# Kernel optimization log

Measured on AMD Instinct MI355X. Metric: run time of the kernel, lower is better.

Reference implementation:

```python
import jax, jax.numpy as jnp
import numpy as np

K = 3
TOPK = 32
TELEPORT = 0.1
LN_EPS = 1e-5


def _block(x, ln_g, ln_b, w1, b1, w2, b2, log_tau, gate):
    residual = x
    # pre: LayerNorm -> Linear -> GELU (exact erf, torch default)
    mu = jnp.mean(x, axis=-1, keepdims=True)
    var = jnp.mean(jnp.square(x - mu), axis=-1, keepdims=True)
    h = (x - mu) * jax.lax.rsqrt(var + LN_EPS) * ln_g + ln_b
    h = jax.nn.gelu(h @ w1 + b1, approximate=False)  # [B, N, H]

    # dynamic cosine adjacency with top-k sparsification
    tau = jnp.maximum(jnp.exp(log_tau), 1e-3)
    xn = h / jnp.maximum(jnp.linalg.norm(h, axis=-1, keepdims=True), 1e-12)
    A = jnp.maximum(jnp.einsum('bnf,bmf->bnm', xn, xn), 0.0)  # [B, N, N]
    B, N, _ = A.shape
    vals, idx = jax.lax.top_k(A, TOPK)  # idx: [B, N, TOPK]
    bi = jnp.arange(B)[:, None, None]
    ni = jnp.arange(N)[None, :, None]
    mask = jnp.zeros(A.shape, dtype=bool).at[bi, ni, idx].set(True)
    I = jnp.eye(N, dtype=A.dtype)
    A = jnp.where(mask, A, 0.0) + I
    A = A / tau

    # teleport + symmetric degree normalization
    A = (1.0 - TELEPORT) * A + TELEPORT * I
    deg = jnp.maximum(A.sum(-1), 1e-6)  # [B, N]
    dm12 = deg ** -0.5
    Ahat = dm12[:, :, None] * A * dm12[:, None, :]

    # Chebyshev propagation
    T0 = h
    outs = [T0]
    if K > 1:
        T1 = jnp.einsum('bnm,bmf->bnf', Ahat, T0)
        outs.append(T1)
    for _ in range(2, K):
        outs.append(2.0 * jnp.einsum('bnm,bmf->bnf', Ahat, outs[-1]) - outs[-2])
    hcat = jnp.concatenate(outs, axis=-1)  # [B, N, H*K]
    y = hcat @ w2 + b2
    return residual + jnp.tanh(gate) * y


def setup_inputs() -> dict:
    key = jax.random.key(0)
    k0, k1, k2 = jax.random.split(key, 3)
    Bsz, N, D, H, O = 4, 4096, 128, 128, 128
    x = jax.random.normal(k0, (Bsz, N, D), dtype=jnp.float32)
    ln_g = jnp.ones((D,), jnp.float32)
    ln_b = jnp.zeros((D,), jnp.float32)
    w1 = jax.random.normal(k1, (D, H), jnp.float32) / np.float32(np.sqrt(D))
    b1 = jnp.zeros((H,), jnp.float32)
    w2 = jax.random.normal(k2, (H * K, O), jnp.float32) / np.float32(np.sqrt(H * K))
    b2 = jnp.zeros((O,), jnp.float32)
    log_tau = jnp.asarray(np.log(0.5), jnp.float32)
    gate = jnp.asarray(0.2, jnp.float32)
    return {"x": x, "ln_g": ln_g, "ln_b": ln_b, "w1": w1, "b1": b1,
            "w2": w2, "b2": b2, "log_tau": log_tau, "gate": gate}


def reference(x, ln_g, ln_b, w1, b1, w2, b2, log_tau, gate):
    return _block(x, ln_g, ln_b, w1, b1, w2, b2, log_tau, gate)
```

## Files before the change

kernel.cpp:

```cpp
#include <hip/hip_runtime.h>
#include <hip/hip_bf16.h>
#include <stdint.h>

#define NB 4
#define NN 4096

using f16x8 = __attribute__((ext_vector_type(8))) _Float16;
using f32x4 = __attribute__((ext_vector_type(4))) float;

__device__ __forceinline__ float wave_sum(float v) {
  #pragma unroll
  for (int o = 32; o > 0; o >>= 1) v += __shfl_xor(v, o, 64);
  return v;
}
__device__ __forceinline__ unsigned short f2h_bits(float f) {
  _Float16 hf = (_Float16)f;
  unsigned short us;
  __builtin_memcpy(&us, &hf, 2);
  return us;
}
__device__ __forceinline__ unsigned pack2h(float lo, float hi) {
  return ((unsigned)f2h_bits(hi) << 16) | (unsigned)f2h_bits(lo);
}

#define INS16(c) do { unsigned t_;                      \
  t_ = max(l0, c);  c = min(l0, c);  l0 = t_;           \
  t_ = max(l1, c);  c = min(l1, c);  l1 = t_;           \
  t_ = max(l2, c);  c = min(l2, c);  l2 = t_;           \
  t_ = max(l3, c);  c = min(l3, c);  l3 = t_;           \
  t_ = max(l4, c);  c = min(l4, c);  l4 = t_;           \
  t_ = max(l5, c);  c = min(l5, c);  l5 = t_;           \
  t_ = max(l6, c);  c = min(l6, c);  l6 = t_;           \
  t_ = max(l7, c);  c = min(l7, c);  l7 = t_;           \
  t_ = max(l8, c);  c = min(l8, c);  l8 = t_;           \
  t_ = max(l9, c);  c = min(l9, c);  l9 = t_;           \
  t_ = max(l10, c); c = min(l10, c); l10 = t_;          \
  t_ = max(l11, c); c = min(l11, c); l11 = t_;          \
  t_ = max(l12, c); c = min(l12, c); l12 = t_;          \
  t_ = max(l13, c); c = min(l13, c); l13 = t_;          \
  t_ = max(l14, c); c = min(l14, c); l14 = t_;          \
  l15 = max(l15, c);                                    \
} while (0)

__global__ __launch_bounds__(128) void k_prepw(
    const float* __restrict__ w1, const float* __restrict__ w2,
    _Float16* __restrict__ w1t16, _Float16* __restrict__ w2t16) {
  int n = blockIdx.x;
  int t = threadIdx.x;
  __shared__ _Float16 v16[128];
  __shared__ float v[384];
  v16[t] = (_Float16)w1[(size_t)t * 128 + n];
  #pragma unroll
  for (int i = 0; i < 3; ++i) v[i * 128 + t] = w2[(size_t)(i * 128 + t) * 128 + n];
  __syncthreads();
  if (t < 16) {
    union { _Float16 hh[8]; uint4 u; } pk;
    #pragma unroll
    for (int j = 0; j < 8; ++j) pk.hh[j] = v16[t * 8 + j];
    *(uint4*)(w1t16 + (size_t)n * 128 + (size_t)(t ^ (n & 7)) * 8) = pk.u;
  }
  if (t < 48) {
    int kc = t >> 4, cl = t & 15;
    union { _Float16 hh[8]; uint4 u; } pk;
    #pragma unroll
    for (int e = 0; e < 8; ++e) pk.hh[e] = (_Float16)v[t * 8 + e];
    *(uint4*)(w2t16 + (size_t)n * 384 + kc * 128 + (size_t)(cl ^ (n & 7)) * 8) = pk.u;
  }
}

__global__ __launch_bounds__(256) void k0_ln(
    const float* __restrict__ x, const float* __restrict__ ln_g,
    const float* __restrict__ ln_b, _Float16* __restrict__ ln16) {
  int lane = threadIdx.x & 63;
  int row = blockIdx.x * 4 + (threadIdx.x >> 6);
  float2 xv = ((const float2*)x)[(size_t)row * 64 + lane];
  float2 gv = ((const float2*)ln_g)[lane];
  float2 bv = ((const float2*)ln_b)[lane];
  float mu = wave_sum(xv.x + xv.y) * (1.0f / 128.0f);
  float dx = xv.x - mu, dy = xv.y - mu;
  float var = wave_sum(dx * dx + dy * dy) * (1.0f / 128.0f);
  float ri = 1.0f / sqrtf(var + 1e-5f);
  float h0 = dx * ri * gv.x + bv.x;
  float h1 = dy * ri * gv.y + bv.y;
  int c = lane >> 2;
  int addr = row * 128 + ((c ^ (row & 7)) << 3) + (lane & 3) * 2;
  *(unsigned*)(ln16 + addr) = pack2h(h0, h1);
}

__global__ __launch_bounds__(256) void k1_mfma(
    const _Float16* __restrict__ ln16, const _Float16* __restrict__ w1t16,
    const float* __restrict__ b1, _Float16* __restrict__ h16,
    _Float16* __restrict__ hn16) {
  __shared__ _Float16 As[64 * 128];
  __shared__ _Float16 Bs[128 * 128];
  int tid = threadIdx.x;
  int lane = tid & 63;
  int wv = tid >> 6;
  int rbase = blockIdx.x * 64;
  #pragma unroll
  for (int i = 0; i < 4; ++i) {
    int idx = tid + 256 * i;
    __builtin_amdgcn_global_load_lds(
        (const __attribute__((address_space(1))) void*)(ln16 + (size_t)rbase * 128 + (size_t)idx * 8),
        (__attribute__((address_space(3))) void*)(As + (size_t)idx * 8), 16, 0, 0);
  }
  #pragma unroll
  for (int i = 0; i < 8; ++i) {
    int idx = tid + 256 * i;
    __builtin_amdgcn_global_load_lds(
        (const __attribute__((address_space(1))) void*)(w1t16 + (size_t)idx * 8),
        (__attribute__((address_space(3))) void*)(Bs + (size_t)idx * 8), 16, 0, 0);
  }
  asm volatile("s_waitcnt vmcnt(0)" ::: "memory");
  __syncthreads();

  int rl = lane & 15, kg = lane >> 4;
  f32x4 acc[8];
  #pragma unroll
  for (int j = 0; j < 8; ++j) acc[j] = (f32x4){0.f, 0.f, 0.f, 0.f};
  #pragma unroll
  for (int kk = 0; kk < 4; ++kk) {
    int cL = kk * 4 + kg;
    int r = wv * 16 + rl;
    f16x8 a = *(const f16x8*)(As + r * 128 + (cL ^ (r & 7)) * 8);
    #pragma unroll
    for (int j = 0; j < 8; ++j) {
      int n = j * 16 + rl;
      f16x8 bf = *(const f16x8*)(Bs + n * 128 + (cL ^ (n & 7)) * 8);
      acc[j] = __builtin_amdgcn_mfma_f32_16x16x32_f16(a, bf, acc[j], 0, 0, 0);
    }
  }
  float ssq[4] = {0.f, 0.f, 0.f, 0.f};
  #pragma unroll
  for (int j = 0; j < 8; ++j) {
    float bv = b1[j * 16 + rl];
    #pragma unroll
    for (int rg = 0; rg < 4; ++rg) {
      float z = acc[j][rg] + bv;
      float g = 0.5f * z * (1.0f + erff(z * 0.70710678118654752440f));
      acc[j][rg] = g;
      ssq[rg] += g * g;
    }
  }
  #pragma unroll
  for (int o = 1; o < 16; o <<= 1)
    #pragma unroll
    for (int rg = 0; rg < 4; ++rg) ssq[rg] += __shfl_xor(ssq[rg], o, 64);
  float rinv[4];
  #pragma unroll
  for (int rg = 0; rg < 4; ++rg) rinv[rg] = 1.0f / fmaxf(sqrtf(ssq[rg]), 1e-12f);

  #pragma unroll
  for (int j = 0; j < 8; ++j) {
    #pragma unroll
    for (int rg = 0; rg < 4; ++rg) {
      float g = acc[j][rg];
      float gp = __shfl_xor(g, 1, 64);
      if ((rl & 1) == 0) {
        int row = rbase + wv * 16 + kg * 4 + rg;
        int col = j * 16 + rl;
        int c = col >> 3;
        int ad = row * 128 + (((c ^ (row & 7))) << 3) + (col & 7);
        *(unsigned*)(h16 + ad) = pack2h(g, gp);
        *(unsigned*)(hn16 + ad) = pack2h(g * rinv[rg], gp * rinv[rg]);
      }
    }
  }
}

__global__ __launch_bounds__(256, 1) void k_scores_topk(
    const _Float16* __restrict__ hn16, int* __restrict__ nidx,
    float* __restrict__ nval, float* __restrict__ dm12,
    const float* __restrict__ p_log_tau) {
  __shared__ _Float16 Qs[64 * 128];
  __shared__ _Float16 Cs[2][128 * 128];
  __shared__ unsigned stk[32 * 256];
  int tid = threadIdx.x;
  int lane = tid & 63;
  int wv = tid >> 6;
  int rl = lane & 15, kg = lane >> 4;
  int blk = blockIdx.x;
  int b = blk >> 6;
  int qbase = (blk & 63) * 64;
  const _Float16* hb = hn16 + (size_t)b * NN * 128;

  #pragma unroll
  for (int i = 0; i < 4; ++i) {
    int idx = tid + 256 * i;
    __builtin_amdgcn_global_load_lds(
        (const __attribute__((address_space(1))) void*)(hb + (size_t)qbase * 128 + (size_t)idx * 8),
        (__attribute__((address_space(3))) void*)(Qs + (size_t)idx * 8), 16, 0, 0);
  }
  #pragma unroll
  for (int i = 0; i < 8; ++i) {
    int idx = tid + 256 * i;
    __builtin_amdgcn_global_load_lds(
        (const __attribute__((address_space(1))) void*)(hb + (size_t)idx * 8),
        (__attribute__((address_space(3))) void*)(Cs[0] + (size_t)idx * 8), 16, 0, 0);
  }
  asm volatile("s_waitcnt vmcnt(0)" ::: "memory");
  __syncthreads();

  int qrow = wv * 16 + rl;
  f16x8 bq[4];
  #pragma unroll
  for (int kk = 0; kk < 4; ++kk)
    bq[kk] = *(const f16x8*)(Qs + qrow * 128 + ((kk * 4 + kg) ^ (qrow & 7)) * 8);

  unsigned l0 = 0, l1 = 0, l2 = 0, l3 = 0, l4 = 0, l5 = 0, l6 = 0, l7 = 0,
           l8 = 0, l9 = 0, l10 = 0, l11 = 0, l12 = 0, l13 = 0, l14 = 0, l15 = 0;
  float thr = 0.0f;

  for (int cb = 0; cb < 32; ++cb) {
    int cur = cb & 1;
    if (cb < 31) {
      const _Float16* csrc = hb + (size_t)(cb + 1) * 128 * 128;
      #pragma unroll
      for (int i = 0; i < 8; ++i) {
        int idx = tid + 256 * i;
        __builtin_amdgcn_global_load_lds(
            (const __attribute__((address_space(1))) void*)(csrc + (size_t)idx * 8),
            (__attribute__((address_space(3))) void*)(Cs[cur ^ 1] + (size_t)idx * 8), 16, 0, 0);
      }
    }
    f32x4 acc[8];
    #pragma unroll
    for (int j = 0; j < 8; ++j) acc[j] = (f32x4){0.f, 0.f, 0.f, 0.f};
    #pragma unroll
    for (int kk = 0; kk < 4; ++kk) {
      #pragma unroll
      for (int j = 0; j < 8; ++j) {
        int mrow = j * 16 + rl;
        f16x8 a = *(const f16x8*)(Cs[cur] + mrow * 128 + ((kk * 4 + kg) ^ (rl & 7)) * 8);
        acc[j] = __builtin_amdgcn_mfma_f32_16x16x32_f16(a, bq[kk], acc[j], 0, 0, 0);
      }
    }
    int cnt = 0;
    int kb = 4095 - (cb * 128 + kg * 4);
    #pragma unroll
    for (int j = 0; j < 8; ++j) {
      float mx = fmaxf(fmaxf(acc[j][0], acc[j][1]), fmaxf(acc[j][2], acc[j][3]));
      if (mx >= thr) {
        #pragma unroll
        for (int rg = 0; rg < 4; ++rg) {
          float v = acc[j][rg];
          if (v >= thr) {
            unsigned key = (__float_as_uint(fmaxf(v, 0.0f)) & 0xFFFFF000u) |
                           (unsigned)(kb - j * 16 - rg);
            stk[cnt * 256 + tid] = key;
            ++cnt;
          }
        }
      }
    }
    for (int i = 0;; ++i) {
      if (__ballot(i < cnt) == 0ull) break;
      unsigned c = (i < cnt) ? stk[i * 256 + tid] : 0u;
      INS16(c);
    }
    thr = __uint_as_float(l15 & 0xFFFFF000u);
    asm volatile("s_waitcnt vmcnt(0)" ::: "memory");
    __syncthreads();
  }

  unsigned sv[8];
  float sum = 0.0f;
  #pragma unroll
  for (int e = 0; e < 32; ++e) {
    unsigned v = l0;
    v = max(v, (unsigned)__shfl_xor((int)v, 16, 64));
    v = max(v, (unsigned)__shfl_xor((int)v, 32, 64));
    if (l0 == v) {
      l0 = l1; l1 = l2; l2 = l3; l3 = l4; l4 = l5; l5 = l6; l6 = l7; l7 = l8;
      l8 = l9; l9 = l10; l10 = l11; l11 = l12; l12 = l13; l13 = l14; l14 = l15; l15 = 0;
    }
    sum += __uint_as_float(v & 0xFFFFF000u);
    if (kg == (e & 3)) sv[e >> 2] = v;
  }
  int grow = b * NN + qbase + qrow;
  #pragma unroll
  for (int s = 0; s < 8; ++s) {
    unsigned v = sv[s];
    nidx[(size_t)grow * 32 + s * 4 + kg] = 4095 - (int)(v & 0xFFFu);
    nval[(size_t)grow * 32 + s * 4 + kg] = __uint_as_float(v & 0xFFFFF000u);
  }
  if (kg == 0) {
    float tau = fmaxf(expf(p_log_tau[0]), 1e-3f);
    float deg = fmaxf(0.9f * ((sum + 1.0f) / tau) + 0.1f, 1e-6f);
    dm12[grow] = 1.0f / sqrtf(deg);
  }
}

__global__ __launch_bounds__(128) void k_cheb1(
    const _Float16* __restrict__ h16, const int* __restrict__ nidx,
    const float* __restrict__ nval, const float* __restrict__ dm12,
    const float* __restrict__ p_log_tau, _Float16* __restrict__ T116) {
  int row = blockIdx.x;
  int b = row >> 12;
  int tid = threadIdx.x;
  __shared__ float cj[32];
  __shared__ int mj[32];
  __shared__ float cdsh;
  float tau = fmaxf(expf(p_log_tau[0]), 1e-3f);
  float scale = 0.9f / tau;
  float dn = dm12[row];
  if (tid < 32) {
    int m = nidx[(size_t)row * 32 + tid];
    cj[tid] = scale * nval[(size_t)row * 32 + tid] * dn * dm12[b * NN + m];
    mj[tid] = m;
  }
  if (tid == 0) cdsh = (scale + 0.1f) * dn * dn;
  __syncthreads();
  int c = tid >> 3, e = tid & 7;
  const _Float16* hb = h16 + (size_t)b * NN * 128;
  float acc = cdsh * (float)h16[(size_t)row * 128 + ((c ^ (row & 7)) << 3) + e];
  #pragma unroll 8
  for (int j = 0; j < 32; ++j) {
    int m = mj[j];
    acc += cj[j] * (float)hb[(size_t)m * 128 + ((c ^ (m & 7)) << 3) + e];
  }
  float p = __shfl_xor(acc, 1, 64);
  if (!(tid & 1))
    *(unsigned*)(T116 + (size_t)row * 128 + ((c ^ (row & 7)) << 3) + e) = pack2h(acc, p);
}

__global__ __launch_bounds__(128) void k_cheb2(
    const _Float16* __restrict__ h16, const _Float16* __restrict__ T116,
    const int* __restrict__ nidx, const float* __restrict__ nval,
    const float* __restrict__ dm12, const float* __restrict__ p_log_tau,
    _Float16* __restrict__ T216) {
  int row = blockIdx.x;
  int b = row >> 12;
  int tid = threadIdx.x;
  __shared__ float cj[32];
  __shared__ int mj[32];
  __shared__ float cdsh;
  float tau = fmaxf(expf(p_log_tau[0]), 1e-3f);
  float scale = 0.9f / tau;
  float dn = dm12[row];
  if (tid < 32) {
    int m = nidx[(size_t)row * 32 + tid];
    cj[tid] = scale * nval[(size_t)row * 32 + tid] * dn * dm12[b * NN + m];
    mj[tid] = m;
  }
  if (tid == 0) cdsh = (scale + 0.1f) * dn * dn;
  __syncthreads();
  int c = tid >> 3, e = tid & 7;
  int sw_own = ((c ^ (row & 7)) << 3) + e;
  const _Float16* T1b = T116 + (size_t)b * NN * 128;
  float a = cdsh * (float)T116[(size_t)row * 128 + sw_own];
  #pragma unroll 8
  for (int j = 0; j < 32; ++j) {
    int m = mj[j];
    a += cj[j] * (float)T1b[(size_t)m * 128 + ((c ^ (m & 7)) << 3) + e];
  }
  float t2 = 2.0f * a - (float)h16[(size_t)row * 128 + sw_own];
  float p = __shfl_xor(t2, 1, 64);
  if (!(tid & 1))
    *(unsigned*)(T216 + (size_t)row * 128 + sw_own) = pack2h(t2, p);
}

__global__ __launch_bounds__(256, 1) void k_out(
    const float* __restrict__ x, const _Float16* __restrict__ h16,
    const _Float16* __restrict__ T116, const _Float16* __restrict__ T216,
    const _Float16* __restrict__ w2t16, const float* __restrict__ b2,
    const float* __restrict__ p_gate, float* __restrict__ out) {
  __shared__ _Float16 As3[3][64 * 128];
  __shared__ _Float16 Bs3[3][128 * 128];
  int tid = threadIdx.x;
  int lane = tid & 63;
  int wv = tid >> 6;
  int rbase = blockIdx.x * 64;
  const _Float16* srcs[3] = {h16, T116, T216};
  #pragma unroll
  for (int kc = 0; kc < 3; ++kc) {
    const _Float16* src = srcs[kc] + (size_t)rbase * 128;
    #pragma unroll
    for (int i = 0; i < 4; ++i) {
      int idx = tid + 256 * i;
      __builtin_amdgcn_global_load_lds(
          (const __attribute__((address_space(1))) void*)(src + (size_t)idx * 8),
          (__attribute__((address_space(3))) void*)(As3[kc] + (size_t)idx * 8), 16, 0, 0);
    }
    #pragma unroll
    for (int i = 0; i < 8; ++i) {
      int idx = tid + 256 * i;
      int n = idx >> 4, cp = idx & 15;
      __builtin_amdgcn_global_load_lds(
          (const __attribute__((address_space(1))) void*)(w2t16 + (size_t)n * 384 + kc * 128 + (size_t)cp * 8),
          (__attribute__((address_space(3))) void*)(Bs3[kc] + (size_t)idx * 8), 16, 0, 0);
    }
  }
  asm volatile("s_waitcnt vmcnt(0)" ::: "memory");
  __syncthreads();

  int rl = lane & 15, kg = lane >> 4;
  f32x4 acc[8];
  #pragma unroll
  for (int j = 0; j < 8; ++j) acc[j] = (f32x4){0.f, 0.f, 0.f, 0.f};
  #pragma unroll
  for (int kc = 0; kc < 3; ++kc) {
    #pragma unroll
    for (int kk = 0; kk < 4; ++kk) {
      int cL = kk * 4 + kg;
      int r = wv * 16 + rl;
      f16x8 a = *(const f16x8*)(As3[kc] + r * 128 + (cL ^ (r & 7)) * 8);
      #pragma unroll
      for (int j = 0; j < 8; ++j) {
        int n = j * 16 + rl;
        f16x8 bf = *(const f16x8*)(Bs3[kc] + n * 128 + (cL ^ (n & 7)) * 8);
        acc[j] = __builtin_amdgcn_mfma_f32_16x16x32_f16(a, bf, acc[j], 0, 0, 0);
      }
    }
  }
  float tg = tanhf(p_gate[0]);
  #pragma unroll
  for (int j = 0; j < 8; ++j) {
    int col = j * 16 + rl;
    float bv = b2[col];
    #pragma unroll
    for (int rg = 0; rg < 4; ++rg) {
      int row = rbase + wv * 16 + kg * 4 + rg;
      out[(size_t)row * 128 + col] =
          x[(size_t)row * 128 + col] + tg * (acc[j][rg] + bv);
    }
  }
}

extern "C" void kernel_launch(void* const* d_in, const int* in_sizes, int n_in,
                              void* d_out, int out_size, void* d_ws, size_t ws_size,
                              hipStream_t stream) {
  (void)in_sizes; (void)n_in; (void)out_size; (void)ws_size;
  const float* x = (const float*)d_in[0];
  const float* ln_g = (const float*)d_in[1];
  const float* ln_b = (const float*)d_in[2];
  const float* w1 = (const float*)d_in[3];
  const float* b1 = (const float*)d_in[4];
  const float* w2 = (const float*)d_in[5];
  const float* b2 = (const float*)d_in[6];
  const float* p_log_tau = (const float*)d_in[7];
  const float* p_gate = (const float*)d_in[8];
  float* out = (float*)d_out;

  char* ws = (char*)d_ws;
  size_t off = 0;
  auto alloc = [&](size_t bytes) -> void* {
    off = (off + 255) & ~(size_t)255;
    void* p = ws + off;
    off += bytes;
    return p;
  };
  _Float16* ln16 = (_Float16*)alloc((size_t)NB * NN * 128 * 2);
  _Float16* h16 = (_Float16*)alloc((size_t)NB * NN * 128 * 2);
  _Float16* hn16 = (_Float16*)alloc((size_t)NB * NN * 128 * 2);
  _Float16* T116 = (_Float16*)alloc((size_t)NB * NN * 128 * 2);
  _Float16* T216 = (_Float16*)alloc((size_t)NB * NN * 128 * 2);
  _Float16* w1t16 = (_Float16*)alloc((size_t)128 * 128 * 2);
  _Float16* w2t16 = (_Float16*)alloc((size_t)128 * 384 * 2);
  int* nidx = (int*)alloc((size_t)NB * NN * 32 * 4);
  float* nval = (float*)alloc((size_t)NB * NN * 32 * 4);
  float* dm12 = (float*)alloc((size_t)NB * NN * 4);

  k_prepw<<<128, 128, 0, stream>>>(w1, w2, w1t16, w2t16);
  k0_ln<<<NB * NN / 4, 256, 0, stream>>>(x, ln_g, ln_b, ln16);
  k1_mfma<<<NB * NN / 64, 256, 0, stream>>>(ln16, w1t16, b1, h16, hn16);
  k_scores_topk<<<NB * 64, 256, 0, stream>>>(hn16, nidx, nval, dm12, p_log_tau);
  k_cheb1<<<NB * NN, 128, 0, stream>>>(h16, nidx, nval, dm12, p_log_tau, T116);
  k_cheb2<<<NB * NN, 128, 0, stream>>>(h16, T116, nidx, nval, dm12, p_log_tau, T216);
  k_out<<<NB * NN / 64, 256, 0, stream>>>(x, h16, T116, T216, w2t16, b2, p_gate, out);
}
```

Before: 202.8 us.

## Split top-k candidate scan across two wave groups and merge lists

The scores/top-k kernel now runs 512 threads per block. Two groups of four waves each scan half of the candidate columns with their own double-buffered LDS tiles, then group 1's per-lane top-16 lists are merged into group 0's through shared memory. Keys now pack an fp16 score above the index, and the pre-filter compares directly against the current 16th-best key rather than a float threshold. This doubles the wave-level parallelism on a grid of only 256 blocks, at the cost of an extra merge step and coarser score precision in the key.

```diff
diff --git a/kernel.cpp b/kernel.cpp
--- a/kernel.cpp
+++ b/kernel.cpp
@@ -12,6 +12,12 @@
   #pragma unroll
   for (int o = 32; o > 0; o >>= 1) v += __shfl_xor(v, o, 64);
   return v;
+}
+__device__ __forceinline__ float h2f_bits(unsigned hb) {
+  unsigned short us = (unsigned short)hb;
+  _Float16 hf;
+  __builtin_memcpy(&hf, &us, 2);
+  return (float)hf;
 }
 __device__ __forceinline__ unsigned short f2h_bits(float f) {
   _Float16 hf = (_Float16)f;
@@ -42,6 +48,11 @@
   l15 = max(l15, c);                                    \
 } while (0)
 
+#define SHIFT_L() do { l0=l1; l1=l2; l2=l3; l3=l4; l4=l5; l5=l6; l6=l7; l7=l8; \
+  l8=l9; l9=l10; l10=l11; l11=l12; l12=l13; l13=l14; l14=l15; l15=0; } while (0)
+#define SHIFT_P() do { p0=p1; p1=p2; p2=p3; p3=p4; p4=p5; p5=p6; p6=p7; p7=p8; \
+  p8=p9; p9=p10; p10=p11; p11=p12; p12=p13; p13=p14; p14=p15; p15=0; } while (0)
+
 __global__ __launch_bounds__(128) void k_prepw(
     const float* __restrict__ w1, const float* __restrict__ w2,
     _Float16* __restrict__ w1t16, _Float16* __restrict__ w2t16) {
@@ -168,40 +179,44 @@
   }
 }
 
-__global__ __launch_bounds__(256, 1) void k_scores_topk(
+__global__ __launch_bounds__(512, 1) void k_scores_topk(
     const _Float16* __restrict__ hn16, int* __restrict__ nidx,
     float* __restrict__ nval, float* __restrict__ dm12,
     const float* __restrict__ p_log_tau) {
   __shared__ _Float16 Qs[64 * 128];
-  __shared__ _Float16 Cs[2][128 * 128];
-  __shared__ unsigned stk[32 * 256];
+  __shared__ _Float16 Cs[2][2][64 * 128];
+  __shared__ unsigned stk[16 * 512];
   int tid = threadIdx.x;
   int lane = tid & 63;
   int wv = tid >> 6;
+  int g = wv >> 2;
+  int wq = wv & 3;
   int rl = lane & 15, kg = lane >> 4;
+  int t = tid & 255;
   int blk = blockIdx.x;
   int b = blk >> 6;
   int qbase = (blk & 63) * 64;
   const _Float16* hb = hn16 + (size_t)b * NN * 128;
 
   #pragma unroll
-  for (int i = 0; i < 4; ++i) {
-    int idx = tid + 256 * i;
+  for (int i = 0; i < 2; ++i) {
+    int idx = tid + 512 * i;
     __builtin_amdgcn_global_load_lds(
         (const __attribute__((address_space(1))) void*)(hb + (size_t)qbase * 128 + (size_t)idx * 8),
         (__attribute__((address_space(3))) void*)(Qs + (size_t)idx * 8), 16, 0, 0);
   }
-  #pragma unroll
-  for (int i = 0; i < 8; ++i) {
-    int idx = tid + 256 * i;
+  const _Float16* cw = hb + (size_t)(g * 2048) * 128;
+  #pragma unroll
+  for (int i = 0; i < 4; ++i) {
+    int idx = t + 256 * i;
     __builtin_amdgcn_global_load_lds(
-        (const __attribute__((address_space(1))) void*)(hb + (size_t)idx * 8),
-        (__attribute__((address_space(3))) void*)(Cs[0] + (size_t)idx * 8), 16, 0, 0);
+        (const __attribute__((address_space(1))) void*)(cw + (size_t)idx * 8),
+        (__attribute__((address_space(3))) void*)(&Cs[g][0][0] + (size_t)idx * 8), 16, 0, 0);
   }
   asm volatile("s_waitcnt vmcnt(0)" ::: "memory");
   __syncthreads();
 
-  int qrow = wv * 16 + rl;
+  int qrow = wq * 16 + rl;
   f16x8 bq[4];
   #pragma unroll
   for (int kk = 0; kk < 4; ++kk)
@@ -209,85 +224,97 @@
 
   unsigned l0 = 0, l1 = 0, l2 = 0, l3 = 0, l4 = 0, l5 = 0, l6 = 0, l7 = 0,
            l8 = 0, l9 = 0, l10 = 0, l11 = 0, l12 = 0, l13 = 0, l14 = 0, l15 = 0;
-  float thr = 0.0f;
 
   for (int cb = 0; cb < 32; ++cb) {
     int cur = cb & 1;
     if (cb < 31) {
-      const _Float16* csrc = hb + (size_t)(cb + 1) * 128 * 128;
+      const _Float16* csrc = cw + (size_t)(cb + 1) * 64 * 128;
       #pragma unroll
-      for (int i = 0; i < 8; ++i) {
-        int idx = tid + 256 * i;
+      for (int i = 0; i < 4; ++i) {
+        int idx = t + 256 * i;
         __builtin_amdgcn_global_load_lds(
             (const __attribute__((address_space(1))) void*)(csrc + (size_t)idx * 8),
-            (__attribute__((address_space(3))) void*)(Cs[cur ^ 1] + (size_t)idx * 8), 16, 0, 0);
+            (__attribute__((address_space(3))) void*)(&Cs[g][cur ^ 1][0] + (size_t)idx * 8), 16, 0, 0);
       }
     }
-    f32x4 acc[8];
-    #pragma unroll
-    for (int j = 0; j < 8; ++j) acc[j] = (f32x4){0.f, 0.f, 0.f, 0.f};
+    f32x4 acc[4];
+    #pragma unroll
+    for (int j = 0; j < 4; ++j) acc[j] = (f32x4){0.f, 0.f, 0.f, 0.f};
     #pragma unroll
     for (int kk = 0; kk < 4; ++kk) {
       #pragma unroll
-      for (int j = 0; j < 8; ++j) {
+      for (int j = 0; j < 4; ++j) {
         int mrow = j * 16 + rl;
-        f16x8 a = *(const f16x8*)(Cs[cur] + mrow * 128 + ((kk * 4 + kg) ^ (rl & 7)) * 8);
+        f16x8 a = *(const f16x8*)(&Cs[g][cur][0] + mrow * 128 + ((kk * 4 + kg) ^ (rl & 7)) * 8);
         acc[j] = __builtin_amdgcn_mfma_f32_16x16x32_f16(a, bq[kk], acc[j], 0, 0, 0);
       }
     }
     int cnt = 0;
-    int kb = 4095 - (cb * 128 + kg * 4);
-    #pragma unroll
-    for (int j = 0; j < 8; ++j) {
-      float mx = fmaxf(fmaxf(acc[j][0], acc[j][1]), fmaxf(acc[j][2], acc[j][3]));
-      if (mx >= thr) {
-        #pragma unroll
-        for (int rg = 0; rg < 4; ++rg) {
-          float v = acc[j][rg];
-          if (v >= thr) {
-            unsigned key = (__float_as_uint(fmaxf(v, 0.0f)) & 0xFFFFF000u) |
-                           (unsigned)(kb - j * 16 - rg);
-            stk[cnt * 256 + tid] = key;
-            ++cnt;
-          }
+    int kb = 4095 - (g * 2048 + cb * 64 + kg * 4);
+    #pragma unroll
+    for (int j = 0; j < 4; ++j) {
+      #pragma unroll
+      for (int rg = 0; rg < 4; ++rg) {
+        float v = fmaxf(acc[j][rg], 0.0f);
+        unsigned key = ((unsigned)f2h_bits(v) << 16) | (unsigned)(kb - j * 16 - rg);
+        if (key > l15) {
+          stk[cnt * 512 + tid] = key;
+          ++cnt;
         }
       }
     }
     for (int i = 0;; ++i) {
       if (__ballot(i < cnt) == 0ull) break;
-      unsigned c = (i < cnt) ? stk[i * 256 + tid] : 0u;
+      unsigned c = (i < cnt) ? stk[i * 512 + tid] : 0u;
       INS16(c);
     }
-    thr = __uint_as_float(l15 & 0xFFFFF000u);
     asm volatile("s_waitcnt vmcnt(0)" ::: "memory");
     __syncthreads();
   }
 
-  unsigned sv[8];
-  float sum = 0.0f;
-  #pragma unroll
-  for (int e = 0; e < 32; ++e) {
-    unsigned v = l0;
-    v = max(v, (unsigned)__shfl_xor((int)v, 16, 64));
-    v = max(v, (unsigned)__shfl_xor((int)v, 32, 64));
-    if (l0 == v) {
-      l0 = l1; l1 = l2; l2 = l3; l3 = l4; l4 = l5; l5 = l6; l6 = l7; l7 = l8;
-      l8 = l9; l9 = l10; l10 = l11; l11 = l12; l12 = l13; l13 = l14; l14 = l15; l15 = 0;
-    }
-    sum += __uint_as_float(v & 0xFFFFF000u);
-    if (kg == (e & 3)) sv[e >> 2] = v;
-  }
-  int grow = b * NN + qbase + qrow;
-  #pragma unroll
-  for (int s = 0; s < 8; ++s) {
-    unsigned v = sv[s];
-    nidx[(size_t)grow * 32 + s * 4 + kg] = 4095 - (int)(v & 0xFFFu);
-    nval[(size_t)grow * 32 + s * 4 + kg] = __uint_as_float(v & 0xFFFFF000u);
-  }
-  if (kg == 0) {
-    float tau = fmaxf(expf(p_log_tau[0]), 1e-3f);
-    float deg = fmaxf(0.9f * ((sum + 1.0f) / tau) + 0.1f, 1e-6f);
-    dm12[grow] = 1.0f / sqrtf(deg);
+  if (g == 1) {
+    unsigned* dst = stk + (((wq * 16 + rl) * 4 + kg) * 16);
+    *(uint4*)(dst + 0)  = (uint4){l0, l1, l2, l3};
+    *(uint4*)(dst + 4)  = (uint4){l4, l5, l6, l7};
+    *(uint4*)(dst + 8)  = (uint4){l8, l9, l10, l11};
+    *(uint4*)(dst + 12) = (uint4){l12, l13, l14, l15};
+  }
+  __syncthreads();
+  if (g == 0) {
+    const unsigned* src = stk + (((wq * 16 + rl) * 4 + kg) * 16);
+    uint4 pa = *(const uint4*)(src + 0);
+    uint4 pb = *(const uint4*)(src + 4);
+    uint4 pc = *(const uint4*)(src + 8);
+    uint4 pd = *(const uint4*)(src + 12);
+    unsigned p0 = pa.x, p1 = pa.y, p2 = pa.z, p3 = pa.w;
+    unsigned p4 = pb.x, p5 = pb.y, p6 = pb.z, p7 = pb.w;
+    unsigned p8 = pc.x, p9 = pc.y, p10 = pc.z, p11 = pc.w;
+    unsigned p12 = pd.x, p13 = pd.y, p14 = pd.z, p15 = pd.w;
+
+    unsigned sv[8];
+    float sum = 0.0f;
+    #pragma unroll
+    for (int e = 0; e < 32; ++e) {
+      unsigned v = max(l0, p0);
+      v = max(v, (unsigned)__shfl_xor((int)v, 16, 64));
+      v = max(v, (unsigned)__shfl_xor((int)v, 32, 64));
+      if (l0 == v) { SHIFT_L(); }
+      else if (p0 == v) { SHIFT_P(); }
+      sum += h2f_bits(v >> 16);
+      if (kg == (e & 3)) sv[e >> 2] = v;
+    }
+    int grow = b * NN + qbase + qrow;
+    #pragma unroll
+    for (int s = 0; s < 8; ++s) {
+      unsigned v = sv[s];
+      nidx[(size_t)grow * 32 + s * 4 + kg] = 4095 - (int)(v & 0xFFFu);
+      nval[(size_t)grow * 32 + s * 4 + kg] = h2f_bits(v >> 16);
+    }
+    if (kg == 0) {
+      float tau = fmaxf(expf(p_log_tau[0]), 1e-3f);
+      float deg = fmaxf(0.9f * ((sum + 1.0f) / tau) + 0.1f, 1e-6f);
+      dm12[grow] = 1.0f / sqrtf(deg);
+    }
   }
 }
 
@@ -464,7 +491,7 @@
   k_prepw<<<128, 128, 0, stream>>>(w1, w2, w1t16, w2t16);
   k0_ln<<<NB * NN / 4, 256, 0, stream>>>(x, ln_g, ln_b, ln16);
   k1_mfma<<<NB * NN / 64, 256, 0, stream>>>(ln16, w1t16, b1, h16, hn16);
-  k_scores_topk<<<NB * 64, 256, 0, stream>>>(hn16, nidx, nval, dm12, p_log_tau);
+  k_scores_topk<<<NB * 64, 512, 0, stream>>>(hn16, nidx, nval, dm12, p_log_tau);
   k_cheb1<<<NB * NN, 128, 0, stream>>>(h16, nidx, nval, dm12, p_log_tau, T116);
   k_cheb2<<<NB * NN, 128, 0, stream>>>(h16, T116, nidx, nval, dm12, p_log_tau, T216);
   k_out<<<NB * NN / 64, 256, 0, stream>>>(x, h16, T116, T216, w2t16, b2, p_gate, out);
```

Result: faster. 177.4 us (-12.5%).
